# Performance work log

Hardware: AMD Instinct MI355X
Metric: run time of the kernel (lower is better)

Reference implementation:

```python
import jax, jax.numpy as jnp
import numpy as np

KS = 3          # deformable kernel size
PAD = 1         # zero padding
N = KS * KS     # sample points per pixel


def conv2d(x, w, b=None, padding=1):
    out = jax.lax.conv_general_dilated(
        x, w, (1, 1), [(padding, padding)] * 2,
        dimension_numbers=('NCHW', 'OIHW', 'NCHW'))
    if b is not None:
        out = out + b[None, :, None, None]
    return out


def setup_inputs() -> dict:
    key = jax.random.key(0)
    k0, k1, k2, k3 = jax.random.split(key, 4)
    B, C, H, W, O = 4, 64, 128, 128, 64
    x = jax.random.normal(k0, (B, C, H, W), jnp.float32)
    # p_conv / m_conv are zero-init in the original; use small random weights
    # so offsets/modulation are non-trivial but sampling stays local.
    w_p = jax.random.normal(k1, (2 * N, C, 3, 3), jnp.float32) * 0.01
    b_p = jnp.zeros((2 * N,), jnp.float32)
    w_m = jax.random.normal(k2, (N, C, 3, 3), jnp.float32) * 0.01
    b_m = jnp.zeros((N,), jnp.float32)
    w_conv = jax.random.normal(k3, (O, C, KS, KS), jnp.float32) / np.sqrt(C * N)
    return {'x': x, 'w_p': w_p, 'b_p': b_p, 'w_m': w_m, 'b_m': b_m, 'w_conv': w_conv}


def reference(x, w_p, b_p, w_m, b_m, w_conv):
    B, C, H, W = x.shape
    offset = conv2d(x, w_p, b_p)              # (B, 2N, H, W): first N rows(x), last N cols(y)
    m = jax.nn.sigmoid(conv2d(x, w_m, b_m))   # (B, N, H, W) modulation
    xp = jnp.pad(x, ((0, 0), (0, 0), (PAD, PAD), (PAD, PAD)))  # zero_padding
    Hp, Wp = H + 2 * PAD, W + 2 * PAD

    # p = p_0 + p_n + offset  (coords in padded image, p_0 starts at 1)
    r = (KS - 1) // 2
    pn_x, pn_y = jnp.meshgrid(jnp.arange(-r, r + 1), jnp.arange(-r, r + 1), indexing='ij')
    pn = jnp.concatenate([pn_x.reshape(-1), pn_y.reshape(-1)]).astype(x.dtype)          # (2N,)
    p0_x, p0_y = jnp.meshgrid(jnp.arange(1, H + 1), jnp.arange(1, W + 1), indexing='ij')
    p0 = jnp.concatenate([jnp.tile(p0_x[None], (N, 1, 1)),
                          jnp.tile(p0_y[None], (N, 1, 1))], 0).astype(x.dtype)           # (2N,H,W)
    p = offset + pn[None, :, None, None] + p0[None]
    p = jnp.moveaxis(p, 1, -1)                # (B,H,W,2N)

    fx = jnp.floor(jax.lax.stop_gradient(p[..., :N]))  # p.detach().floor()
    fy = jnp.floor(jax.lax.stop_gradient(p[..., N:]))
    q_lt_x = jnp.clip(fx, 0, Hp - 1).astype(jnp.int32)
    q_lt_y = jnp.clip(fy, 0, Wp - 1).astype(jnp.int32)
    q_rb_x = jnp.clip(fx + 1, 0, Hp - 1).astype(jnp.int32)
    q_rb_y = jnp.clip(fy + 1, 0, Wp - 1).astype(jnp.int32)
    px = jnp.clip(p[..., :N], 0, Hp - 1)
    py = jnp.clip(p[..., N:], 0, Wp - 1)

    # bilinear kernel weights (same algebra as torch version)
    g_lt = (1 + (q_lt_x - px)) * (1 + (q_lt_y - py))
    g_rb = (1 - (q_rb_x - px)) * (1 - (q_rb_y - py))
    g_lb = (1 + (q_lt_x - px)) * (1 - (q_rb_y - py))
    g_rt = (1 - (q_rb_x - px)) * (1 + (q_lt_y - py))

    xf = xp.reshape(B, C, Hp * Wp)

    def gather(qx, qy):
        idx = (qx * Wp + qy).reshape(B, 1, -1)                      # (B,1,H*W*N)
        return jnp.take_along_axis(xf, idx, axis=2).reshape(B, C, H, W, N)

    x_off = (g_lt[:, None] * gather(q_lt_x, q_lt_y)
             + g_rb[:, None] * gather(q_rb_x, q_rb_y)
             + g_lb[:, None] * gather(q_lt_x, q_rb_y)
             + g_rt[:, None] * gather(q_rb_x, q_lt_y))               # (B,C,H,W,N)

    x_off = x_off * jnp.moveaxis(m, 1, -1)[:, None]                  # modulation (DCNv2)

    # _reshape_x_offset + conv(kernel=ks, stride=ks) == einsum over the N samples
    out = jnp.einsum('bchwk,ock->bohw', x_off,
                     w_conv.reshape(w_conv.shape[0], C, N))
    return out
```

## Files before the change

kernel.cpp:

```cpp
#include <hip/hip_runtime.h>
#include <hip/hip_bf16.h>

#define BB 4
#define CC 64
#define HH 128
#define WW 128
#define OO 64
#define NN 9
#define HW 16384
#define HP 130
#define WP 130

#define WPMB_F  0
#define BPM_OFF 9216
#define WCB_F   9248
#define XT_F    27680
#define PX_OFF  2124832
#define PSZ     589824

typedef __attribute__((ext_vector_type(8))) short s8v;
typedef __attribute__((ext_vector_type(8))) unsigned short u8v;
typedef __attribute__((ext_vector_type(4))) float f4v;

__device__ __forceinline__ unsigned short f2bu(float f) {
    unsigned int b = __float_as_uint(f);
    return (unsigned short)((b + 0x7FFFu + ((b >> 16) & 1u)) >> 16);
}
__device__ __forceinline__ float bu2f(unsigned short u) {
    return __uint_as_float(((unsigned int)u) << 16);
}

__global__ void k_prep(const float* __restrict__ wp,
                       const float* __restrict__ bp,
                       const float* __restrict__ wm,
                       const float* __restrict__ bm,
                       const float* __restrict__ wcv,
                       float* __restrict__ ws) {
    int tid = blockIdx.x * blockDim.x + threadIdx.x;
    if (tid < 18432) {
        int r = tid / 576;
        int kk = tid % 576;
        int kt = kk >> 6;
        int c = kk & 63;
        int dy = kt / 3, dx = kt % 3;
        float v = 0.f;
        if (r < 18)       v = wp[((r * 64 + c) * 3 + dy) * 3 + dx];
        else if (r < 27)  v = wm[(((r - 18) * 64 + c) * 3 + dy) * 3 + dx];
        ((unsigned short*)(ws + WPMB_F))[tid] = f2bu(v);
    } else if (tid < 18459) {
        int i = tid - 18432;
        ws[BPM_OFF + i] = (i < 18) ? bp[i] : bm[i - 18];
    } else if (tid >= 20480 && tid < 20480 + 36864) {
        int d = tid - 20480;
        int o = d / 576;
        int kk = d % 576;
        int kt = kk >> 6;
        int c = kk & 63;
        ((unsigned short*)(ws + WCB_F))[o * 576 + kk] = f2bu(wcv[(o * 64 + c) * 9 + kt]);
    }
}

__global__ void __launch_bounds__(256) k_xt(const float* __restrict__ x,
                                            float* __restrict__ ws) {
    __shared__ unsigned short tile[64][66];
    int blk = blockIdx.x;
    int b = blk >> 8;
    int hw0 = (blk & 255) * 64;
    int t = threadIdx.x;
    unsigned short* xt = (unsigned short*)(ws + XT_F);

#pragma unroll
    for (int p = 0; p < 16; p++) {
        int c = p * 4 + (t >> 6);
        int i = t & 63;
        tile[c][i] = f2bu(x[((size_t)(b * 64 + c)) * HW + hw0 + i]);
    }
    __syncthreads();
#pragma unroll
    for (int p = 0; p < 16; p++) {
        int i = p * 4 + (t >> 6);
        int c = t & 63;
        xt[((size_t)(b * HW + hw0 + i)) * 64 + c] = tile[c][i];
    }
}

__global__ void __launch_bounds__(256) k_off(const float* __restrict__ ws,
                                             float* __restrict__ wsout) {
    __shared__ unsigned short Awld[32 * 72];
    __shared__ unsigned short Bld[64 * 72];

    int t = threadIdx.x;
    int lane = t & 63;
    int wid = t >> 6;
    int ln15 = lane & 15;
    int quad = lane >> 4;

    int blk = blockIdx.x;
    int b = blk >> 8;
    int hw0 = (blk & 255) * 64;

    const unsigned short* wpmb = (const unsigned short*)(ws + WPMB_F);
    const unsigned short* xtb = (const unsigned short*)(ws + XT_F) + (size_t)b * HW * 64;
    const float* bpm = ws + BPM_OFF;

    int aq_row = t >> 3, aq_g = t & 7;
    int bq_pix = t & 63, bq_half = t >> 6;
    int ph = (hw0 + bq_pix) >> 7;
    int pw = (hw0 + bq_pix) & 127;

    f4v acc[2];
    acc[0] = (f4v){0.f, 0.f, 0.f, 0.f};
    acc[1] = (f4v){0.f, 0.f, 0.f, 0.f};

#pragma unroll 1
    for (int kt = 0; kt < 9; kt++) {
        int dy = kt / 3, dx = kt % 3;
        __syncthreads();
        {
            u8v av = *(const u8v*)(wpmb + aq_row * 576 + kt * 64 + aq_g * 8);
            *(u8v*)(&Awld[aq_row * 72 + aq_g * 8]) = av;
        }
        {
            int h2 = ph + dy - 1, w2 = pw + dx - 1;
            bool val = ((unsigned)h2 < 128u) && ((unsigned)w2 < 128u);
            u8v z = (u8v){0, 0, 0, 0, 0, 0, 0, 0};
            u8v e0 = z, e1 = z;
            if (val) {
                const unsigned short* src = xtb + ((size_t)(h2 * 128 + w2)) * 64 + bq_half * 16;
                e0 = *(const u8v*)(src);
                e1 = *(const u8v*)(src + 8);
            }
            *(u8v*)(&Bld[bq_pix * 72 + bq_half * 16]) = e0;
            *(u8v*)(&Bld[bq_pix * 72 + bq_half * 16 + 8]) = e1;
        }
        __syncthreads();

#pragma unroll
        for (int ks = 0; ks < 2; ks++) {
            s8v bf = *(const s8v*)(&Bld[(wid * 16 + ln15) * 72 + ks * 32 + quad * 8]);
#pragma unroll
            for (int mt = 0; mt < 2; mt++) {
                s8v af = *(const s8v*)(&Awld[(mt * 16 + ln15) * 72 + ks * 32 + quad * 8]);
                acc[mt] = __builtin_amdgcn_mfma_f32_16x16x32_bf16(af, bf, acc[mt], 0, 0, 0);
            }
        }
    }

    int p = hw0 + wid * 16 + ln15;
    int h = p >> 7, w = p & 127;
    float* pxA = wsout + PX_OFF;
    float* pyA = pxA + PSZ;
    float* mmA = pyA + PSZ;
#pragma unroll
    for (int mt = 0; mt < 2; mt++) {
#pragma unroll
        for (int r = 0; r < 4; r++) {
            int oc = mt * 16 + quad * 4 + r;
            if (oc < 27) {
                float v = acc[mt][r] + bpm[oc];
                if (oc < 9) {
                    int ki = oc / 3;
                    pxA[((size_t)b * NN + oc) * HW + p] = v + (float)(ki - 1) + (float)(h + 1);
                } else if (oc < 18) {
                    int k = oc - 9;
                    int kj = k % 3;
                    pyA[((size_t)b * NN + k) * HW + p] = v + (float)(kj - 1) + (float)(w + 1);
                } else {
                    int k = oc - 18;
                    mmA[((size_t)b * NN + k) * HW + p] = 1.f / (1.f + __expf(-v));
                }
            }
        }
    }
}

__global__ void __launch_bounds__(256) k_gemm(const float* __restrict__ ws,
                                              float* __restrict__ out) {
    __shared__ unsigned short Ald[64 * 72];
    __shared__ unsigned short Sld[64 * 72];

    int t = threadIdx.x;
    int lane = t & 63;
    int wid = t >> 6;
    int ln15 = lane & 15;
    int quad = lane >> 4;

    int blk = blockIdx.x;
    int b = blk >> 8;
    int hw0 = (blk & 255) * 64;

    const unsigned short* wcb = (const unsigned short*)(ws + WCB_F);
    const unsigned short* xtb = (const unsigned short*)(ws + XT_F) + (size_t)b * HW * 64;
    const float* pxA = ws + PX_OFF;
    const float* pyA = pxA + PSZ;
    const float* mmA = pyA + PSZ;

    int p_loc = t >> 2;
    int cq = t & 3;

    f4v acc[4];
#pragma unroll
    for (int mt = 0; mt < 4; mt++) acc[mt] = (f4v){0.f, 0.f, 0.f, 0.f};

#pragma unroll 1
    for (int kt = 0; kt < 9; kt++) {
        size_t pidx = ((size_t)b * NN + kt) * HW + hw0 + p_loc;
        float px = pxA[pidx];
        float py = pyA[pidx];
        float mk = mmA[pidx];

        float fx = floorf(px), fy = floorf(py);
        float pxc = fminf(fmaxf(px, 0.f), (float)(HP - 1));
        float pyc = fminf(fmaxf(py, 0.f), (float)(WP - 1));
        int qltx = (int)fminf(fmaxf(fx, 0.f), (float)(HP - 1));
        int qlty = (int)fminf(fmaxf(fy, 0.f), (float)(WP - 1));
        int qrbx = (int)fminf(fmaxf(fx + 1.f, 0.f), (float)(HP - 1));
        int qrby = (int)fminf(fmaxf(fy + 1.f, 0.f), (float)(WP - 1));

        float gltx = 1.f + ((float)qltx - pxc);
        float glty = 1.f + ((float)qlty - pyc);
        float grbx = 1.f - ((float)qrbx - pxc);
        float grby = 1.f - ((float)qrby - pyc);

        bool vlx = (qltx >= 1) && (qltx <= HH);
        bool vly = (qlty >= 1) && (qlty <= WW);
        bool vrx = (qrbx >= 1) && (qrbx <= HH);
        bool vry = (qrby >= 1) && (qrby <= WW);
        float g0 = (vlx && vly) ? gltx * glty * mk : 0.f;
        float g1 = (vrx && vry) ? grbx * grby * mk : 0.f;
        float g2 = (vlx && vry) ? gltx * grby * mk : 0.f;
        float g3 = (vrx && vly) ? grbx * glty * mk : 0.f;

        int xlt = min(max(qltx - 1, 0), HH - 1);
        int ylt = min(max(qlty - 1, 0), WW - 1);
        int xrb = min(max(qrbx - 1, 0), HH - 1);
        int yrb = min(max(qrby - 1, 0), WW - 1);
        size_t i0 = (size_t)(xlt * WW + ylt) * 64;
        size_t i1 = (size_t)(xrb * WW + yrb) * 64;
        size_t i2 = (size_t)(xlt * WW + yrb) * 64;
        size_t i3 = (size_t)(xrb * WW + ylt) * 64;

        __syncthreads();
        {
            int row = t >> 2, g = t & 3;
            const unsigned short* src = wcb + row * 576 + kt * 64 + g * 16;
            *(u8v*)(&Ald[row * 72 + g * 16]) = *(const u8v*)(src);
            *(u8v*)(&Ald[row * 72 + g * 16 + 8]) = *(const u8v*)(src + 8);
        }
        {
            int cbase = cq * 16;
            const unsigned short* s0 = xtb + i0 + cbase;
            const unsigned short* s1 = xtb + i1 + cbase;
            const unsigned short* s2 = xtb + i2 + cbase;
            const unsigned short* s3 = xtb + i3 + cbase;
            u8v e0a = *(const u8v*)(s0), e0b = *(const u8v*)(s0 + 8);
            u8v e1a = *(const u8v*)(s1), e1b = *(const u8v*)(s1 + 8);
            u8v e2a = *(const u8v*)(s2), e2b = *(const u8v*)(s2 + 8);
            u8v e3a = *(const u8v*)(s3), e3b = *(const u8v*)(s3 + 8);
            u8v sva, svb;
#pragma unroll
            for (int j = 0; j < 8; j++) {
                float va = g0 * bu2f(e0a[j]) + g1 * bu2f(e1a[j])
                         + g2 * bu2f(e2a[j]) + g3 * bu2f(e3a[j]);
                float vb = g0 * bu2f(e0b[j]) + g1 * bu2f(e1b[j])
                         + g2 * bu2f(e2b[j]) + g3 * bu2f(e3b[j]);
                sva[j] = f2bu(va);
                svb[j] = f2bu(vb);
            }
            *(u8v*)(&Sld[p_loc * 72 + cbase]) = sva;
            *(u8v*)(&Sld[p_loc * 72 + cbase + 8]) = svb;
        }
        __syncthreads();

#pragma unroll
        for (int ks = 0; ks < 2; ks++) {
            s8v bf = *(const s8v*)(&Sld[(wid * 16 + ln15) * 72 + ks * 32 + quad * 8]);
#pragma unroll
            for (int mt = 0; mt < 4; mt++) {
                s8v af = *(const s8v*)(&Ald[(mt * 16 + ln15) * 72 + ks * 32 + quad * 8]);
                acc[mt] = __builtin_amdgcn_mfma_f32_16x16x32_bf16(af, bf, acc[mt], 0, 0, 0);
            }
        }
    }

    int pix = hw0 + wid * 16 + ln15;
    float* ob = out + (size_t)b * (OO * HW) + pix;
#pragma unroll
    for (int mt = 0; mt < 4; mt++) {
#pragma unroll
        for (int r = 0; r < 4; r++) {
            ob[(size_t)(mt * 16 + quad * 4 + r) * HW] = acc[mt][r];
        }
    }
}

extern "C" void kernel_launch(void* const* d_in, const int* in_sizes, int n_in,
                              void* d_out, int out_size, void* d_ws, size_t ws_size,
                              hipStream_t stream) {
    const float* x   = (const float*)d_in[0];
    const float* wp  = (const float*)d_in[1];
    const float* bp  = (const float*)d_in[2];
    const float* wm  = (const float*)d_in[3];
    const float* bm  = (const float*)d_in[4];
    const float* wcv = (const float*)d_in[5];
    float* ws = (float*)d_ws;
    float* out = (float*)d_out;

    hipLaunchKernelGGL(k_prep, dim3(224), dim3(256), 0, stream, wp, bp, wm, bm, wcv, ws);
    hipLaunchKernelGGL(k_xt, dim3(1024), dim3(256), 0, stream, x, ws);
    hipLaunchKernelGGL(k_off, dim3(1024), dim3(256), 0, stream, ws, ws);
    hipLaunchKernelGGL(k_gemm, dim3(1024), dim3(256), 0, stream, ws, out);
}
```

Baseline: 122.1 us.

## Double-buffer LDS tiles in offset and gather GEMMs; merge prep into transpose kernel

Both the offset conv GEMM and the deformable gather GEMM now use two LDS buffers. Each loop iteration loads and computes the next k-tile (including the bilinear gather and the offset/modulation prefetch) while MFMAs run on the current tile, and each iteration needs only one barrier instead of two. The weight-prep kernel is folded into the transpose kernel as extra blocks, which removes one launch. The cost is doubled LDS use and higher register pressure, which may lower occupancy.

```diff
diff --git a/kernel.cpp b/kernel.cpp
--- a/kernel.cpp
+++ b/kernel.cpp
@@ -30,45 +30,44 @@
     return __uint_as_float(((unsigned int)u) << 16);
 }
 
-__global__ void k_prep(const float* __restrict__ wp,
-                       const float* __restrict__ bp,
-                       const float* __restrict__ wm,
-                       const float* __restrict__ bm,
-                       const float* __restrict__ wcv,
-                       float* __restrict__ ws) {
-    int tid = blockIdx.x * blockDim.x + threadIdx.x;
-    if (tid < 18432) {
-        int r = tid / 576;
-        int kk = tid % 576;
-        int kt = kk >> 6;
-        int c = kk & 63;
-        int dy = kt / 3, dx = kt % 3;
-        float v = 0.f;
-        if (r < 18)       v = wp[((r * 64 + c) * 3 + dy) * 3 + dx];
-        else if (r < 27)  v = wm[(((r - 18) * 64 + c) * 3 + dy) * 3 + dx];
-        ((unsigned short*)(ws + WPMB_F))[tid] = f2bu(v);
-    } else if (tid < 18459) {
-        int i = tid - 18432;
-        ws[BPM_OFF + i] = (i < 18) ? bp[i] : bm[i - 18];
-    } else if (tid >= 20480 && tid < 20480 + 36864) {
-        int d = tid - 20480;
-        int o = d / 576;
-        int kk = d % 576;
-        int kt = kk >> 6;
-        int c = kk & 63;
-        ((unsigned short*)(ws + WCB_F))[o * 576 + kk] = f2bu(wcv[(o * 64 + c) * 9 + kt]);
-    }
-}
-
-__global__ void __launch_bounds__(256) k_xt(const float* __restrict__ x,
-                                            float* __restrict__ ws) {
+__global__ void __launch_bounds__(256) k_pxt(const float* __restrict__ x,
+                                             const float* __restrict__ wp,
+                                             const float* __restrict__ bp,
+                                             const float* __restrict__ wm,
+                                             const float* __restrict__ bm,
+                                             const float* __restrict__ wcv,
+                                             float* __restrict__ ws) {
     __shared__ unsigned short tile[64][66];
     int blk = blockIdx.x;
+    int t = threadIdx.x;
+    if (blk >= 1024) {
+        int tid = (blk - 1024) * 256 + t;
+        if (tid < 18432) {
+            int r = tid / 576;
+            int kk = tid % 576;
+            int kt = kk >> 6;
+            int c = kk & 63;
+            int dy = kt / 3, dx = kt % 3;
+            float v = 0.f;
+            if (r < 18)       v = wp[((r * 64 + c) * 3 + dy) * 3 + dx];
+            else if (r < 27)  v = wm[(((r - 18) * 64 + c) * 3 + dy) * 3 + dx];
+            ((unsigned short*)(ws + WPMB_F))[tid] = f2bu(v);
+        } else if (tid < 18459) {
+            int i = tid - 18432;
+            ws[BPM_OFF + i] = (i < 18) ? bp[i] : bm[i - 18];
+        } else if (tid >= 20480) {
+            int d = tid - 20480;
+            int o = d / 576;
+            int kk = d % 576;
+            int kt = kk >> 6;
+            int c = kk & 63;
+            ((unsigned short*)(ws + WCB_F))[o * 576 + kk] = f2bu(wcv[(o * 64 + c) * 9 + kt]);
+        }
+        return;
+    }
     int b = blk >> 8;
     int hw0 = (blk & 255) * 64;
-    int t = threadIdx.x;
     unsigned short* xt = (unsigned short*)(ws + XT_F);
-
 #pragma unroll
     for (int p = 0; p < 16; p++) {
         int c = p * 4 + (t >> 6);
@@ -86,8 +85,8 @@
 
 __global__ void __launch_bounds__(256) k_off(const float* __restrict__ ws,
                                              float* __restrict__ wsout) {
-    __shared__ unsigned short Awld[32 * 72];
-    __shared__ unsigned short Bld[64 * 72];
+    __shared__ unsigned short Awld[2][32 * 72];
+    __shared__ unsigned short Bld[2][64 * 72];
 
     int t = threadIdx.x;
     int lane = t & 63;
@@ -112,38 +111,55 @@
     acc[0] = (f4v){0.f, 0.f, 0.f, 0.f};
     acc[1] = (f4v){0.f, 0.f, 0.f, 0.f};
 
+    const u8v z = (u8v){0, 0, 0, 0, 0, 0, 0, 0};
+
+    {
+        u8v av = *(const u8v*)(wpmb + aq_row * 576 + aq_g * 8);
+        int h2 = ph - 1, w2 = pw - 1;
+        bool val = ((unsigned)h2 < 128u) && ((unsigned)w2 < 128u);
+        u8v e0 = z, e1 = z;
+        if (val) {
+            const unsigned short* src = xtb + ((size_t)(h2 * 128 + w2)) * 64 + bq_half * 16;
+            e0 = *(const u8v*)(src);
+            e1 = *(const u8v*)(src + 8);
+        }
+        *(u8v*)(&Awld[0][aq_row * 72 + aq_g * 8]) = av;
+        *(u8v*)(&Bld[0][bq_pix * 72 + bq_half * 16]) = e0;
+        *(u8v*)(&Bld[0][bq_pix * 72 + bq_half * 16 + 8]) = e1;
+    }
+    __syncthreads();
+
 #pragma unroll 1
     for (int kt = 0; kt < 9; kt++) {
-        int dy = kt / 3, dx = kt % 3;
-        __syncthreads();
-        {
-            u8v av = *(const u8v*)(wpmb + aq_row * 576 + kt * 64 + aq_g * 8);
-            *(u8v*)(&Awld[aq_row * 72 + aq_g * 8]) = av;
-        }
-        {
+        int cur = kt & 1, nxt = cur ^ 1;
+        u8v an = z, n0 = z, n1 = z;
+        if (kt < 8) {
+            int k2 = kt + 1;
+            an = *(const u8v*)(wpmb + aq_row * 576 + k2 * 64 + aq_g * 8);
+            int dy = k2 / 3, dx = k2 % 3;
             int h2 = ph + dy - 1, w2 = pw + dx - 1;
             bool val = ((unsigned)h2 < 128u) && ((unsigned)w2 < 128u);
-            u8v z = (u8v){0, 0, 0, 0, 0, 0, 0, 0};
-            u8v e0 = z, e1 = z;
             if (val) {
                 const unsigned short* src = xtb + ((size_t)(h2 * 128 + w2)) * 64 + bq_half * 16;
-                e0 = *(const u8v*)(src);
-                e1 = *(const u8v*)(src + 8);
-            }
-            *(u8v*)(&Bld[bq_pix * 72 + bq_half * 16]) = e0;
-            *(u8v*)(&Bld[bq_pix * 72 + bq_half * 16 + 8]) = e1;
+                n0 = *(const u8v*)(src);
+                n1 = *(const u8v*)(src + 8);
+            }
+        }
+#pragma unroll
+        for (int ks = 0; ks < 2; ks++) {
+            s8v bf = *(const s8v*)(&Bld[cur][(wid * 16 + ln15) * 72 + ks * 32 + quad * 8]);
+#pragma unroll
+            for (int mt = 0; mt < 2; mt++) {
+                s8v af = *(const s8v*)(&Awld[cur][(mt * 16 + ln15) * 72 + ks * 32 + quad * 8]);
+                acc[mt] = __builtin_amdgcn_mfma_f32_16x16x32_bf16(af, bf, acc[mt], 0, 0, 0);
+            }
+        }
+        if (kt < 8) {
+            *(u8v*)(&Awld[nxt][aq_row * 72 + aq_g * 8]) = an;
+            *(u8v*)(&Bld[nxt][bq_pix * 72 + bq_half * 16]) = n0;
+            *(u8v*)(&Bld[nxt][bq_pix * 72 + bq_half * 16 + 8]) = n1;
         }
         __syncthreads();
-
-#pragma unroll
-        for (int ks = 0; ks < 2; ks++) {
-            s8v bf = *(const s8v*)(&Bld[(wid * 16 + ln15) * 72 + ks * 32 + quad * 8]);
-#pragma unroll
-            for (int mt = 0; mt < 2; mt++) {
-                s8v af = *(const s8v*)(&Awld[(mt * 16 + ln15) * 72 + ks * 32 + quad * 8]);
-                acc[mt] = __builtin_amdgcn_mfma_f32_16x16x32_bf16(af, bf, acc[mt], 0, 0, 0);
-            }
-        }
     }
 
     int p = hw0 + wid * 16 + ln15;
@@ -176,8 +192,8 @@
 
 __global__ void __launch_bounds__(256) k_gemm(const float* __restrict__ ws,
                                               float* __restrict__ out) {
-    __shared__ unsigned short Ald[64 * 72];
-    __shared__ unsigned short Sld[64 * 72];
+    __shared__ unsigned short Ald[2][64 * 72];
+    __shared__ unsigned short Sld[2][64 * 72];
 
     int t = threadIdx.x;
     int lane = t & 63;
@@ -197,18 +213,18 @@
 
     int p_loc = t >> 2;
     int cq = t & 3;
+    int cbase = cq * 16;
+    int arow = t >> 2, ag = t & 3;
 
     f4v acc[4];
 #pragma unroll
     for (int mt = 0; mt < 4; mt++) acc[mt] = (f4v){0.f, 0.f, 0.f, 0.f};
 
-#pragma unroll 1
-    for (int kt = 0; kt < 9; kt++) {
-        size_t pidx = ((size_t)b * NN + kt) * HW + hw0 + p_loc;
-        float px = pxA[pidx];
-        float py = pyA[pidx];
-        float mk = mmA[pidx];
-
+    size_t pbase = (size_t)b * NN * HW + (size_t)(hw0 + p_loc);
+
+    auto desc = [&](float px, float py, float mk,
+                    float& g0, float& g1, float& g2, float& g3,
+                    int& o0, int& o1, int& o2, int& o3) {
         float fx = floorf(px), fy = floorf(py);
         float pxc = fminf(fmaxf(px, 0.f), (float)(HP - 1));
         float pyc = fminf(fmaxf(py, 0.f), (float)(WP - 1));
@@ -226,37 +242,79 @@
         bool vly = (qlty >= 1) && (qlty <= WW);
         bool vrx = (qrbx >= 1) && (qrbx <= HH);
         bool vry = (qrby >= 1) && (qrby <= WW);
-        float g0 = (vlx && vly) ? gltx * glty * mk : 0.f;
-        float g1 = (vrx && vry) ? grbx * grby * mk : 0.f;
-        float g2 = (vlx && vry) ? gltx * grby * mk : 0.f;
-        float g3 = (vrx && vly) ? grbx * glty * mk : 0.f;
+        g0 = (vlx && vly) ? gltx * glty * mk : 0.f;
+        g1 = (vrx && vry) ? grbx * grby * mk : 0.f;
+        g2 = (vlx && vry) ? gltx * grby * mk : 0.f;
+        g3 = (vrx && vly) ? grbx * glty * mk : 0.f;
 
         int xlt = min(max(qltx - 1, 0), HH - 1);
         int ylt = min(max(qlty - 1, 0), WW - 1);
         int xrb = min(max(qrbx - 1, 0), HH - 1);
         int yrb = min(max(qrby - 1, 0), WW - 1);
-        size_t i0 = (size_t)(xlt * WW + ylt) * 64;
-        size_t i1 = (size_t)(xrb * WW + yrb) * 64;
-        size_t i2 = (size_t)(xlt * WW + yrb) * 64;
-        size_t i3 = (size_t)(xrb * WW + ylt) * 64;
-
-        __syncthreads();
-        {
-            int row = t >> 2, g = t & 3;
-            const unsigned short* src = wcb + row * 576 + kt * 64 + g * 16;
-            *(u8v*)(&Ald[row * 72 + g * 16]) = *(const u8v*)(src);
-            *(u8v*)(&Ald[row * 72 + g * 16 + 8]) = *(const u8v*)(src + 8);
-        }
-        {
-            int cbase = cq * 16;
-            const unsigned short* s0 = xtb + i0 + cbase;
-            const unsigned short* s1 = xtb + i1 + cbase;
-            const unsigned short* s2 = xtb + i2 + cbase;
-            const unsigned short* s3 = xtb + i3 + cbase;
-            u8v e0a = *(const u8v*)(s0), e0b = *(const u8v*)(s0 + 8);
-            u8v e1a = *(const u8v*)(s1), e1b = *(const u8v*)(s1 + 8);
-            u8v e2a = *(const u8v*)(s2), e2b = *(const u8v*)(s2 + 8);
-            u8v e3a = *(const u8v*)(s3), e3b = *(const u8v*)(s3 + 8);
+        o0 = (xlt * WW + ylt) * 64 + cbase;
+        o1 = (xrb * WW + yrb) * 64 + cbase;
+        o2 = (xlt * WW + yrb) * 64 + cbase;
+        o3 = (xrb * WW + ylt) * 64 + cbase;
+    };
+
+    float pxn, pyn, mkn;
+    {
+        float px = pxA[pbase], py = pyA[pbase], mk = mmA[pbase];
+        pxn = pxA[pbase + HW]; pyn = pyA[pbase + HW]; mkn = mmA[pbase + HW];
+        float g0, g1, g2, g3; int o0, o1, o2, o3;
+        desc(px, py, mk, g0, g1, g2, g3, o0, o1, o2, o3);
+        u8v e0a = *(const u8v*)(xtb + o0), e0b = *(const u8v*)(xtb + o0 + 8);
+        u8v e1a = *(const u8v*)(xtb + o1), e1b = *(const u8v*)(xtb + o1 + 8);
+        u8v e2a = *(const u8v*)(xtb + o2), e2b = *(const u8v*)(xtb + o2 + 8);
+        u8v e3a = *(const u8v*)(xtb + o3), e3b = *(const u8v*)(xtb + o3 + 8);
+        u8v a0 = *(const u8v*)(wcb + arow * 576 + ag * 16);
+        u8v a1 = *(const u8v*)(wcb + arow * 576 + ag * 16 + 8);
+        u8v sva, svb;
+#pragma unroll
+        for (int j = 0; j < 8; j++) {
+            float va = g0 * bu2f(e0a[j]) + g1 * bu2f(e1a[j])
+                     + g2 * bu2f(e2a[j]) + g3 * bu2f(e3a[j]);
+            float vb = g0 * bu2f(e0b[j]) + g1 * bu2f(e1b[j])
+                     + g2 * bu2f(e2b[j]) + g3 * bu2f(e3b[j]);
+            sva[j] = f2bu(va);
+            svb[j] = f2bu(vb);
+        }
+        *(u8v*)(&Sld[0][p_loc * 72 + cbase]) = sva;
+        *(u8v*)(&Sld[0][p_loc * 72 + cbase + 8]) = svb;
+        *(u8v*)(&Ald[0][arow * 72 + ag * 16]) = a0;
+        *(u8v*)(&Ald[0][arow * 72 + ag * 16 + 8]) = a1;
+    }
+    __syncthreads();
+
+#pragma unroll 1
+    for (int kt = 0; kt < 9; kt++) {
+        int cur = kt & 1, nxt = cur ^ 1;
+        float g0 = 0.f, g1 = 0.f, g2 = 0.f, g3 = 0.f;
+        u8v e0a, e0b, e1a, e1b, e2a, e2b, e3a, e3b, a0, a1;
+        if (kt < 8) {
+            int o0, o1, o2, o3;
+            desc(pxn, pyn, mkn, g0, g1, g2, g3, o0, o1, o2, o3);
+            e0a = *(const u8v*)(xtb + o0); e0b = *(const u8v*)(xtb + o0 + 8);
+            e1a = *(const u8v*)(xtb + o1); e1b = *(const u8v*)(xtb + o1 + 8);
+            e2a = *(const u8v*)(xtb + o2); e2b = *(const u8v*)(xtb + o2 + 8);
+            e3a = *(const u8v*)(xtb + o3); e3b = *(const u8v*)(xtb + o3 + 8);
+            a0 = *(const u8v*)(wcb + arow * 576 + (kt + 1) * 64 + ag * 16);
+            a1 = *(const u8v*)(wcb + arow * 576 + (kt + 1) * 64 + ag * 16 + 8);
+            if (kt < 7) {
+                size_t pn = pbase + (size_t)(kt + 2) * HW;
+                pxn = pxA[pn]; pyn = pyA[pn]; mkn = mmA[pn];
+            }
+        }
+#pragma unroll
+        for (int ks = 0; ks < 2; ks++) {
+            s8v bf = *(const s8v*)(&Sld[cur][(wid * 16 + ln15) * 72 + ks * 32 + quad * 8]);
+#pragma unroll
+            for (int mt = 0; mt < 4; mt++) {
+                s8v af = *(const s8v*)(&Ald[cur][(mt * 16 + ln15) * 72 + ks * 32 + quad * 8]);
+                acc[mt] = __builtin_amdgcn_mfma_f32_16x16x32_bf16(af, bf, acc[mt], 0, 0, 0);
+            }
+        }
+        if (kt < 8) {
             u8v sva, svb;
 #pragma unroll
             for (int j = 0; j < 8; j++) {
@@ -267,20 +325,12 @@
                 sva[j] = f2bu(va);
                 svb[j] = f2bu(vb);
             }
-            *(u8v*)(&Sld[p_loc * 72 + cbase]) = sva;
-            *(u8v*)(&Sld[p_loc * 72 + cbase + 8]) = svb;
+            *(u8v*)(&Sld[nxt][p_loc * 72 + cbase]) = sva;
+            *(u8v*)(&Sld[nxt][p_loc * 72 + cbase + 8]) = svb;
+            *(u8v*)(&Ald[nxt][arow * 72 + ag * 16]) = a0;
+            *(u8v*)(&Ald[nxt][arow * 72 + ag * 16 + 8]) = a1;
         }
         __syncthreads();
-
-#pragma unroll
-        for (int ks = 0; ks < 2; ks++) {
-            s8v bf = *(const s8v*)(&Sld[(wid * 16 + ln15) * 72 + ks * 32 + quad * 8]);
-#pragma unroll
-            for (int mt = 0; mt < 4; mt++) {
-                s8v af = *(const s8v*)(&Ald[(mt * 16 + ln15) * 72 + ks * 32 + quad * 8]);
-                acc[mt] = __builtin_amdgcn_mfma_f32_16x16x32_bf16(af, bf, acc[mt], 0, 0, 0);
-            }
-        }
     }
 
     int pix = hw0 + wid * 16 + ln15;
@@ -306,8 +356,7 @@
     float* ws = (float*)d_ws;
     float* out = (float*)d_out;
 
-    hipLaunchKernelGGL(k_prep, dim3(224), dim3(256), 0, stream, wp, bp, wm, bm, wcv, ws);
-    hipLaunchKernelGGL(k_xt, dim3(1024), dim3(256), 0, stream, x, ws);
+    hipLaunchKernelGGL(k_pxt, dim3(1248), dim3(256), 0, stream, x, wp, bp, wm, bm, wcv, ws);
     hipLaunchKernelGGL(k_off, dim3(1024), dim3(256), 0, stream, ws, ws);
     hipLaunchKernelGGL(k_gemm, dim3(1024), dim3(256), 0, stream, ws, out);
 }
```

New measurement: 116.0 us. 1.05x faster.
